# Optimization experiments

Hardware: AMD Instinct MI355X
Metric: run time of the kernel (lower is better)

Reference implementation:

```python
import jax, jax.numpy as jnp
import numpy as np

H = 16  # hidden/input size
EPS = 1e-5


def _lstm_layer(xs, W_ih, W_hh, b_ih, b_hh):
    """xs: [T, B, in]. Returns (ys [T,B,H], h_final [B,H]). PyTorch gate order i,f,g,o."""
    B = xs.shape[1]
    h0 = jnp.zeros((B, H), xs.dtype)
    c0 = jnp.zeros((B, H), xs.dtype)
    bias = b_ih + b_hh  # [4H]

    def step(carry, x_t):
        h, c = carry
        gates = x_t @ W_ih.T + h @ W_hh.T + bias  # [B, 4H]
        i, f, g, o = jnp.split(gates, 4, axis=-1)
        i = jax.nn.sigmoid(i)
        f = jax.nn.sigmoid(f)
        g = jnp.tanh(g)
        o = jax.nn.sigmoid(o)
        c = f * c + i * g
        h = o * jnp.tanh(c)
        return (h, c), h

    (h_fin, _), ys = jax.lax.scan(step, (h0, c0), xs)
    return ys, h_fin


def setup_inputs() -> dict:
    key = jax.random.key(0)
    ks = jax.random.split(key, 12)
    s = 1.0 / np.sqrt(H)  # PyTorch LSTM/Linear init scale
    B, T = 4096, 512
    x = jax.random.normal(ks[0], (B, T, H), dtype=jnp.float32)
    u = lambda k, shp: jax.random.uniform(k, shp, jnp.float32, -s, s)
    return {
        "x": x,
        "W_ih0": u(ks[1], (4 * H, H)), "W_hh0": u(ks[2], (4 * H, H)),
        "b_ih0": u(ks[3], (4 * H,)), "b_hh0": u(ks[4], (4 * H,)),
        "W_ih1": u(ks[5], (4 * H, H)), "W_hh1": u(ks[6], (4 * H, H)),
        "b_ih1": u(ks[7], (4 * H,)), "b_hh1": u(ks[8], (4 * H,)),
        "W_proj": u(ks[9], (H, H)), "b_proj": u(ks[10], (H,)),
        "ln_gamma": jnp.ones((H,), jnp.float32), "ln_beta": jnp.zeros((H,), jnp.float32),
    }


def reference(x, W_ih0, W_hh0, b_ih0, b_hh0, W_ih1, W_hh1, b_ih1, b_hh1,
              W_proj, b_proj, ln_gamma, ln_beta):
    xs = jnp.transpose(x, (1, 0, 2))  # [T, B, H] time-major for scan
    ys, _ = _lstm_layer(xs, W_ih0, W_hh0, b_ih0, b_hh0)
    _, h_n = _lstm_layer(ys, W_ih1, W_hh1, b_ih1, b_hh1)  # h_n[-1] == layer-2 final h
    z = h_n @ W_proj.T + b_proj  # [B, H]
    mu = jnp.mean(z, axis=-1, keepdims=True)
    var = jnp.mean(jnp.square(z - mu), axis=-1, keepdims=True)
    z = (z - mu) * jax.lax.rsqrt(var + EPS) * ln_gamma + ln_beta
    return jnp.tanh(z)
```

## Files before the change

### kernel.cpp

```cpp
#include <hip/hip_runtime.h>
#include <cstddef>

#define HH 16
#define TT 512
#define STG 16
#define NSTG (TT / STG)
#define LOG2E 1.44269504088896340736f

typedef float v2f __attribute__((ext_vector_type(2)));
typedef float v4f __attribute__((ext_vector_type(4)));

static __device__ __forceinline__ float fexp2(float x){ return __builtin_amdgcn_exp2f(x); }
static __device__ __forceinline__ float frcp (float x){ return __builtin_amdgcn_rcpf(x); }
static __device__ __forceinline__ float frsq (float x){ return __builtin_amdgcn_rsqf(x); }

static __device__ __forceinline__ float ftanh(float c){
    return frcp(1.0f + fexp2(c * (-2.0f*LOG2E))) * 2.0f - 1.0f;
}

#if __has_builtin(__builtin_amdgcn_mov_dpp)
template<int CTRL>
static __device__ __forceinline__ float qb(float v){
    return __builtin_bit_cast(float,
        __builtin_amdgcn_mov_dpp(__builtin_bit_cast(int,v), CTRL, 0xF, 0xF, true));
}
#else
template<int CTRL>
static __device__ __forceinline__ float qb(float v){
    return __builtin_bit_cast(float,
        __builtin_amdgcn_update_dpp(0, __builtin_bit_cast(int,v), CTRL, 0xF, 0xF, true));
}
#endif

static __device__ __forceinline__ v2f pkfma(v2f a, v2f b, v2f c){
    return __builtin_elementwise_fma(a, b, c);
}

static __device__ __forceinline__ void dot16_acc(const v4f* a, const v4f* w, v2f& s0, v2f& s1){
    s0 = pkfma(a[0].lo, w[0].lo, s0);  s1 = pkfma(a[0].hi, w[0].hi, s1);
    s0 = pkfma(a[1].lo, w[1].lo, s0);  s1 = pkfma(a[1].hi, w[1].hi, s1);
    s0 = pkfma(a[2].lo, w[2].lo, s0);  s1 = pkfma(a[2].hi, w[2].hi, s1);
    s0 = pkfma(a[3].lo, w[3].lo, s0);  s1 = pkfma(a[3].hi, w[3].hi, s1);
}

static __device__ __forceinline__ void ld4(v4f* dst, const float* p){
    const v4f* q = (const v4f*)p;
    dst[0] = q[0]; dst[1] = q[1]; dst[2] = q[2]; dst[3] = q[3];
}

__global__ __launch_bounds__(256, 4) void lstm_fused_kernel(
    const float* __restrict__ x,
    const float* __restrict__ W_ih0, const float* __restrict__ W_hh0,
    const float* __restrict__ b_ih0, const float* __restrict__ b_hh0,
    const float* __restrict__ W_ih1, const float* __restrict__ W_hh1,
    const float* __restrict__ b_ih1, const float* __restrict__ b_hh1,
    const float* __restrict__ W_proj, const float* __restrict__ b_proj,
    const float* __restrict__ ln_g, const float* __restrict__ ln_b,
    float* __restrict__ out)
{
    const int lane = threadIdx.x & 63;
    const int wave = threadIdx.x >> 6;
    const int b    = blockIdx.x * 4 + wave;

    const int g   = lane & 3;
    const int k   = lane >> 2;
    const int row = g * HH + k;

    __shared__ float sh[4 * 544];
    float* xb0 = sh + wave * 544;
    float* xb1 = xb0 + 256;
    float* h1w = xb1 + 256;
    float* h2w = h1w + 16;

    const bool  isg   = (g == 2);
    const float sc_in = isg ? (-2.0f * LOG2E) : (-LOG2E);

    v4f wih0[4], whh0[4], wih1[4], whh1[4];
#pragma unroll
    for (int q = 0; q < 4; ++q) {
        wih0[q] = ((const v4f*)(W_ih0 + row * HH))[q] * sc_in;
        whh0[q] = ((const v4f*)(W_hh0 + row * HH))[q] * sc_in;
        wih1[q] = ((const v4f*)(W_ih1 + row * HH))[q] * sc_in;
        whh1[q] = ((const v4f*)(W_hh1 + row * HH))[q] * sc_in;
    }
    const float bias0 = (b_ih0[row] + b_hh0[row]) * sc_in;
    const float bias1 = (b_ih1[row] + b_hh1[row]) * sc_in;

    const float* xg = x + (size_t)b * TT * HH;

    v4f xs = *(const v4f*)(xg + lane * 4);
    *(v4f*)(xb0 + lane * 4) = xs;
    xs = *(const v4f*)(xg + 256 + lane * 4);

    v4f xa[4];
    ld4(xa, xb0);

    float cs1, cs2 = 0.0f;
    v4f h1a[4], h2a[4];
#pragma unroll
    for (int q = 0; q < 4; ++q) h2a[q] = (v4f)(0.f);

    {
        v2f p0 = {bias0, 0.f}, p1 = {0.f, 0.f};
        dot16_acc(xa, wih0, p0, p1);
        v2f ps = p0 + p1;
        float a1 = ps.x + ps.y;
        float r1 = frcp(1.0f + fexp2(a1));
        float i1 = qb<0x00>(r1), g1 = qb<0xAA>(r1), o1 = qb<0xFF>(r1);
        float gs1 = __builtin_fmaf(g1, -4.0f*LOG2E, 2.0f*LOG2E);
        cs1 = i1 * gs1;
        float h1n = o1 * (frcp(1.0f + fexp2(cs1)) * 2.0f - 1.0f);
        h1w[k] = h1n;
        ld4(h1a, h1w);
        ld4(xa, xb0 + HH);
    }

    for (int s = 0; s < NSTG; ++s) {
        float* cur = (s & 1) ? xb1 : xb0;
        float* nxt = (s & 1) ? xb0 : xb1;

        *(v4f*)(nxt + lane * 4) = xs;
        const int sp = (s + 2 < NSTG) ? (s + 2) : (NSTG - 1);
        xs = *(const v4f*)(xg + (size_t)sp * 256 + lane * 4);

#pragma unroll
        for (int ti = 0; ti < STG; ++ti) {
            v2f p0 = {bias0, 0.f}, p1 = {0.f, 0.f};
            dot16_acc(xa, wih0, p0, p1);
            dot16_acc(h1a, whh0, p0, p1);
            v2f ps = p0 + p1;
            float a1 = ps.x + ps.y;
            float r1 = frcp(1.0f + fexp2(a1));
            float i1 = qb<0x00>(r1), f1 = qb<0x55>(r1);
            float g1 = qb<0xAA>(r1), o1 = qb<0xFF>(r1);
            float gs1 = __builtin_fmaf(g1, -4.0f*LOG2E, 2.0f*LOG2E);
            cs1 = __builtin_fmaf(f1, cs1, i1 * gs1);
            float h1n = o1 * (frcp(1.0f + fexp2(cs1)) * 2.0f - 1.0f);
            h1w[k] = h1n;

            v2f q0 = {bias1, 0.f}, q1 = {0.f, 0.f};
            dot16_acc(h1a, wih1, q0, q1);

            ld4(h1a, h1w);
            ld4(xa, (ti <= 13) ? (cur + (ti + 2) * HH) : (nxt + (ti - 14) * HH));

            dot16_acc(h2a, whh1, q0, q1);
            v2f qs = q0 + q1;
            float a2 = qs.x + qs.y;
            float r2 = frcp(1.0f + fexp2(a2));
            float i2 = qb<0x00>(r2), f2 = qb<0x55>(r2);
            float g2 = qb<0xAA>(r2), o2 = qb<0xFF>(r2);
            float gs2 = __builtin_fmaf(g2, -4.0f*LOG2E, 2.0f*LOG2E);
            cs2 = __builtin_fmaf(f2, cs2, i2 * gs2);
            float h2n = o2 * (frcp(1.0f + fexp2(cs2)) * 2.0f - 1.0f);
            h2w[k] = h2n;
            ld4(h2a, h2w);
        }
    }

    const int u = lane & 15;
    v4f wp[4];
#pragma unroll
    for (int q = 0; q < 4; ++q) wp[q] = ((const v4f*)(W_proj + u * HH))[q];
    v2f z0 = {0.f, 0.f}, z1 = {0.f, 0.f};
    dot16_acc(h2a, wp, z0, z1);
    v2f zs = z0 + z1;
    float z = b_proj[u] + zs.x + zs.y;

    float sacc = z;
    sacc += __shfl_xor(sacc, 1); sacc += __shfl_xor(sacc, 2);
    sacc += __shfl_xor(sacc, 4); sacc += __shfl_xor(sacc, 8);
    const float mu = sacc * (1.0f / 16.0f);

    const float d = z - mu;
    float q2 = d * d;
    q2 += __shfl_xor(q2, 1); q2 += __shfl_xor(q2, 2);
    q2 += __shfl_xor(q2, 4); q2 += __shfl_xor(q2, 8);
    const float var = q2 * (1.0f / 16.0f);

    const float rs  = frsq(var + 1e-5f);
    const float y   = d * rs * ln_g[u] + ln_b[u];
    const float res = ftanh(y);

    if (lane < 16) out[(size_t)b * HH + lane] = res;
}

extern "C" void kernel_launch(void* const* d_in, const int* in_sizes, int n_in,
                              void* d_out, int out_size, void* d_ws, size_t ws_size,
                              hipStream_t stream) {
    const float* x      = (const float*)d_in[0];
    const float* W_ih0  = (const float*)d_in[1];
    const float* W_hh0  = (const float*)d_in[2];
    const float* b_ih0  = (const float*)d_in[3];
    const float* b_hh0  = (const float*)d_in[4];
    const float* W_ih1  = (const float*)d_in[5];
    const float* W_hh1  = (const float*)d_in[6];
    const float* b_ih1  = (const float*)d_in[7];
    const float* b_hh1  = (const float*)d_in[8];
    const float* W_proj = (const float*)d_in[9];
    const float* b_proj = (const float*)d_in[10];
    const float* ln_g   = (const float*)d_in[11];
    const float* ln_b   = (const float*)d_in[12];
    float* out = (float*)d_out;

    const int B = in_sizes[0] / (TT * HH);
    dim3 grid(B / 4), block(256);
    hipLaunchKernelGGL(lstm_fused_kernel, grid, block, 0, stream,
                       x, W_ih0, W_hh0, b_ih0, b_hh0,
                       W_ih1, W_hh1, b_ih1, b_hh1,
                       W_proj, b_proj, ln_g, ln_b, out);
}
```

Baseline: 472.2 us.

## Process two batch sequences per wave to interleave independent LSTM recurrences

Each wavefront now advances two batch elements' two-layer LSTM recurrences in lockstep, doubling shared-memory staging and register state per wave and halving the grid. The goal is to fill the long serial dependency chain of each timestep (dot products, exp/rcp, DPP broadcasts, LDS round trips) with independent work from the second sequence. In exchange, register pressure rises (launch bounds lowered) and the number of resident waves per SIMD drops, so latency hiding shifts from wave switching to in-wave ILP.

Result: no change. 478.8 us (+1.4%).

```diff
diff --git a/kernel.cpp b/kernel.cpp
--- a/kernel.cpp
+++ b/kernel.cpp
@@ -48,7 +48,7 @@
     dst[0] = q[0]; dst[1] = q[1]; dst[2] = q[2]; dst[3] = q[3];
 }
 
-__global__ __launch_bounds__(256, 4) void lstm_fused_kernel(
+__global__ __launch_bounds__(256, 2) void lstm_fused_kernel(
     const float* __restrict__ x,
     const float* __restrict__ W_ih0, const float* __restrict__ W_hh0,
     const float* __restrict__ b_ih0, const float* __restrict__ b_hh0,
@@ -60,17 +60,20 @@
 {
     const int lane = threadIdx.x & 63;
     const int wave = threadIdx.x >> 6;
-    const int b    = blockIdx.x * 4 + wave;
+    const int bA   = blockIdx.x * 8 + wave * 2;
+    const int bB   = bA + 1;
 
     const int g   = lane & 3;
     const int k   = lane >> 2;
     const int row = g * HH + k;
 
-    __shared__ float sh[4 * 544];
-    float* xb0 = sh + wave * 544;
-    float* xb1 = xb0 + 256;
-    float* h1w = xb1 + 256;
-    float* h2w = h1w + 16;
+    __shared__ float sh[8 * 544];
+    float* shA  = sh + (wave * 2 + 0) * 544;
+    float* shB  = sh + (wave * 2 + 1) * 544;
+    float* xb0A = shA;        float* xb0B = shB;
+    float* xb1A = shA + 256;  float* xb1B = shB + 256;
+    float* h1wA = shA + 512;  float* h1wB = shB + 512;
+    float* h2wA = shA + 528;  float* h2wB = shB + 528;
 
     const bool  isg   = (g == 2);
     const float sc_in = isg ? (-2.0f * LOG2E) : (-LOG2E);
@@ -86,75 +89,112 @@
     const float bias0 = (b_ih0[row] + b_hh0[row]) * sc_in;
     const float bias1 = (b_ih1[row] + b_hh1[row]) * sc_in;
 
-    const float* xg = x + (size_t)b * TT * HH;
-
-    v4f xs = *(const v4f*)(xg + lane * 4);
-    *(v4f*)(xb0 + lane * 4) = xs;
-    xs = *(const v4f*)(xg + 256 + lane * 4);
-
-    v4f xa[4];
-    ld4(xa, xb0);
-
-    float cs1, cs2 = 0.0f;
-    v4f h1a[4], h2a[4];
-#pragma unroll
-    for (int q = 0; q < 4; ++q) h2a[q] = (v4f)(0.f);
+    const float* xgA = x + (size_t)bA * TT * HH;
+    const float* xgB = x + (size_t)bB * TT * HH;
+
+    v4f xsA = *(const v4f*)(xgA + lane * 4);
+    v4f xsB = *(const v4f*)(xgB + lane * 4);
+    *(v4f*)(xb0A + lane * 4) = xsA;
+    *(v4f*)(xb0B + lane * 4) = xsB;
+    xsA = *(const v4f*)(xgA + 256 + lane * 4);
+    xsB = *(const v4f*)(xgB + 256 + lane * 4);
+
+    v4f xaA[4], xaB[4];
+    ld4(xaA, xb0A);
+    ld4(xaB, xb0B);
+
+    float cs1A, cs2A = 0.0f;
+    float cs1B, cs2B = 0.0f;
+    v4f h1aA[4], h2aA[4], h1aB[4], h2aB[4];
+#pragma unroll
+    for (int q = 0; q < 4; ++q) { h2aA[q] = (v4f)(0.f); h2aB[q] = (v4f)(0.f); }
 
     {
-        v2f p0 = {bias0, 0.f}, p1 = {0.f, 0.f};
-        dot16_acc(xa, wih0, p0, p1);
-        v2f ps = p0 + p1;
-        float a1 = ps.x + ps.y;
-        float r1 = frcp(1.0f + fexp2(a1));
-        float i1 = qb<0x00>(r1), g1 = qb<0xAA>(r1), o1 = qb<0xFF>(r1);
-        float gs1 = __builtin_fmaf(g1, -4.0f*LOG2E, 2.0f*LOG2E);
-        cs1 = i1 * gs1;
-        float h1n = o1 * (frcp(1.0f + fexp2(cs1)) * 2.0f - 1.0f);
-        h1w[k] = h1n;
-        ld4(h1a, h1w);
-        ld4(xa, xb0 + HH);
+        v2f p0A = {bias0, 0.f}, p1A = {0.f, 0.f};
+        v2f p0B = {bias0, 0.f}, p1B = {0.f, 0.f};
+        dot16_acc(xaA, wih0, p0A, p1A);
+        dot16_acc(xaB, wih0, p0B, p1B);
+        v2f psA = p0A + p1A;               v2f psB = p0B + p1B;
+        float a1A = psA.x + psA.y;         float a1B = psB.x + psB.y;
+        float r1A = frcp(1.0f + fexp2(a1A));
+        float r1B = frcp(1.0f + fexp2(a1B));
+        float i1A = qb<0x00>(r1A), g1A = qb<0xAA>(r1A), o1A = qb<0xFF>(r1A);
+        float i1B = qb<0x00>(r1B), g1B = qb<0xAA>(r1B), o1B = qb<0xFF>(r1B);
+        float gs1A = __builtin_fmaf(g1A, -4.0f*LOG2E, 2.0f*LOG2E);
+        float gs1B = __builtin_fmaf(g1B, -4.0f*LOG2E, 2.0f*LOG2E);
+        cs1A = i1A * gs1A;                 cs1B = i1B * gs1B;
+        float h1nA = o1A * (frcp(1.0f + fexp2(cs1A)) * 2.0f - 1.0f);
+        float h1nB = o1B * (frcp(1.0f + fexp2(cs1B)) * 2.0f - 1.0f);
+        h1wA[k] = h1nA;                    h1wB[k] = h1nB;
+        ld4(h1aA, h1wA);                   ld4(h1aB, h1wB);
+        ld4(xaA, xb0A + HH);               ld4(xaB, xb0B + HH);
     }
 
     for (int s = 0; s < NSTG; ++s) {
-        float* cur = (s & 1) ? xb1 : xb0;
-        float* nxt = (s & 1) ? xb0 : xb1;
-
-        *(v4f*)(nxt + lane * 4) = xs;
+        float* curA = (s & 1) ? xb1A : xb0A;  float* nxtA = (s & 1) ? xb0A : xb1A;
+        float* curB = (s & 1) ? xb1B : xb0B;  float* nxtB = (s & 1) ? xb0B : xb1B;
+
+        *(v4f*)(nxtA + lane * 4) = xsA;
+        *(v4f*)(nxtB + lane * 4) = xsB;
         const int sp = (s + 2 < NSTG) ? (s + 2) : (NSTG - 1);
-        xs = *(const v4f*)(xg + (size_t)sp * 256 + lane * 4);
+        xsA = *(const v4f*)(xgA + (size_t)sp * 256 + lane * 4);
+        xsB = *(const v4f*)(xgB + (size_t)sp * 256 + lane * 4);
 
 #pragma unroll
         for (int ti = 0; ti < STG; ++ti) {
-            v2f p0 = {bias0, 0.f}, p1 = {0.f, 0.f};
-            dot16_acc(xa, wih0, p0, p1);
-            dot16_acc(h1a, whh0, p0, p1);
-            v2f ps = p0 + p1;
-            float a1 = ps.x + ps.y;
-            float r1 = frcp(1.0f + fexp2(a1));
-            float i1 = qb<0x00>(r1), f1 = qb<0x55>(r1);
-            float g1 = qb<0xAA>(r1), o1 = qb<0xFF>(r1);
-            float gs1 = __builtin_fmaf(g1, -4.0f*LOG2E, 2.0f*LOG2E);
-            cs1 = __builtin_fmaf(f1, cs1, i1 * gs1);
-            float h1n = o1 * (frcp(1.0f + fexp2(cs1)) * 2.0f - 1.0f);
-            h1w[k] = h1n;
-
-            v2f q0 = {bias1, 0.f}, q1 = {0.f, 0.f};
-            dot16_acc(h1a, wih1, q0, q1);
-
-            ld4(h1a, h1w);
-            ld4(xa, (ti <= 13) ? (cur + (ti + 2) * HH) : (nxt + (ti - 14) * HH));
-
-            dot16_acc(h2a, whh1, q0, q1);
-            v2f qs = q0 + q1;
-            float a2 = qs.x + qs.y;
-            float r2 = frcp(1.0f + fexp2(a2));
-            float i2 = qb<0x00>(r2), f2 = qb<0x55>(r2);
-            float g2 = qb<0xAA>(r2), o2 = qb<0xFF>(r2);
-            float gs2 = __builtin_fmaf(g2, -4.0f*LOG2E, 2.0f*LOG2E);
-            cs2 = __builtin_fmaf(f2, cs2, i2 * gs2);
-            float h2n = o2 * (frcp(1.0f + fexp2(cs2)) * 2.0f - 1.0f);
-            h2w[k] = h2n;
-            ld4(h2a, h2w);
+            v2f p0A = {bias0, 0.f}, p1A = {0.f, 0.f};
+            v2f p0B = {bias0, 0.f}, p1B = {0.f, 0.f};
+            dot16_acc(xaA, wih0, p0A, p1A);
+            dot16_acc(xaB, wih0, p0B, p1B);
+            dot16_acc(h1aA, whh0, p0A, p1A);
+            dot16_acc(h1aB, whh0, p0B, p1B);
+            v2f psA = p0A + p1A;              v2f psB = p0B + p1B;
+            float a1A = psA.x + psA.y;        float a1B = psB.x + psB.y;
+            float r1A = frcp(1.0f + fexp2(a1A));
+            float r1B = frcp(1.0f + fexp2(a1B));
+            float i1A = qb<0x00>(r1A), f1A = qb<0x55>(r1A);
+            float g1A = qb<0xAA>(r1A), o1A = qb<0xFF>(r1A);
+            float i1B = qb<0x00>(r1B), f1B = qb<0x55>(r1B);
+            float g1B = qb<0xAA>(r1B), o1B = qb<0xFF>(r1B);
+            float gs1A = __builtin_fmaf(g1A, -4.0f*LOG2E, 2.0f*LOG2E);
+            float gs1B = __builtin_fmaf(g1B, -4.0f*LOG2E, 2.0f*LOG2E);
+            cs1A = __builtin_fmaf(f1A, cs1A, i1A * gs1A);
+            cs1B = __builtin_fmaf(f1B, cs1B, i1B * gs1B);
+            float h1nA = o1A * (frcp(1.0f + fexp2(cs1A)) * 2.0f - 1.0f);
+            float h1nB = o1B * (frcp(1.0f + fexp2(cs1B)) * 2.0f - 1.0f);
+            h1wA[k] = h1nA;
+            h1wB[k] = h1nB;
+
+            v2f q0A = {bias1, 0.f}, q1A = {0.f, 0.f};
+            v2f q0B = {bias1, 0.f}, q1B = {0.f, 0.f};
+            dot16_acc(h1aA, wih1, q0A, q1A);
+            dot16_acc(h1aB, wih1, q0B, q1B);
+
+            ld4(h1aA, h1wA);
+            ld4(h1aB, h1wB);
+            ld4(xaA, (ti <= 13) ? (curA + (ti + 2) * HH) : (nxtA + (ti - 14) * HH));
+            ld4(xaB, (ti <= 13) ? (curB + (ti + 2) * HH) : (nxtB + (ti - 14) * HH));
+
+            dot16_acc(h2aA, whh1, q0A, q1A);
+            dot16_acc(h2aB, whh1, q0B, q1B);
+            v2f qsA = q0A + q1A;              v2f qsB = q0B + q1B;
+            float a2A = qsA.x + qsA.y;        float a2B = qsB.x + qsB.y;
+            float r2A = frcp(1.0f + fexp2(a2A));
+            float r2B = frcp(1.0f + fexp2(a2B));
+            float i2A = qb<0x00>(r2A), f2A = qb<0x55>(r2A);
+            float g2A = qb<0xAA>(r2A), o2A = qb<0xFF>(r2A);
+            float i2B = qb<0x00>(r2B), f2B = qb<0x55>(r2B);
+            float g2B = qb<0xAA>(r2B), o2B = qb<0xFF>(r2B);
+            float gs2A = __builtin_fmaf(g2A, -4.0f*LOG2E, 2.0f*LOG2E);
+            float gs2B = __builtin_fmaf(g2B, -4.0f*LOG2E, 2.0f*LOG2E);
+            cs2A = __builtin_fmaf(f2A, cs2A, i2A * gs2A);
+            cs2B = __builtin_fmaf(f2B, cs2B, i2B * gs2B);
+            float h2nA = o2A * (frcp(1.0f + fexp2(cs2A)) * 2.0f - 1.0f);
+            float h2nB = o2B * (frcp(1.0f + fexp2(cs2B)) * 2.0f - 1.0f);
+            h2wA[k] = h2nA;
+            h2wB[k] = h2nB;
+            ld4(h2aA, h2wA);
+            ld4(h2aB, h2wB);
         }
     }
 
@@ -162,27 +202,41 @@
     v4f wp[4];
 #pragma unroll
     for (int q = 0; q < 4; ++q) wp[q] = ((const v4f*)(W_proj + u * HH))[q];
-    v2f z0 = {0.f, 0.f}, z1 = {0.f, 0.f};
-    dot16_acc(h2a, wp, z0, z1);
-    v2f zs = z0 + z1;
-    float z = b_proj[u] + zs.x + zs.y;
-
-    float sacc = z;
-    sacc += __shfl_xor(sacc, 1); sacc += __shfl_xor(sacc, 2);
-    sacc += __shfl_xor(sacc, 4); sacc += __shfl_xor(sacc, 8);
-    const float mu = sacc * (1.0f / 16.0f);
-
-    const float d = z - mu;
-    float q2 = d * d;
-    q2 += __shfl_xor(q2, 1); q2 += __shfl_xor(q2, 2);
-    q2 += __shfl_xor(q2, 4); q2 += __shfl_xor(q2, 8);
-    const float var = q2 * (1.0f / 16.0f);
-
-    const float rs  = frsq(var + 1e-5f);
-    const float y   = d * rs * ln_g[u] + ln_b[u];
-    const float res = ftanh(y);
-
-    if (lane < 16) out[(size_t)b * HH + lane] = res;
+    const float lg = ln_g[u], lb = ln_b[u], bp = b_proj[u];
+
+    v2f z0A = {0.f, 0.f}, z1A = {0.f, 0.f};
+    v2f z0B = {0.f, 0.f}, z1B = {0.f, 0.f};
+    dot16_acc(h2aA, wp, z0A, z1A);
+    dot16_acc(h2aB, wp, z0B, z1B);
+    v2f zsA = z0A + z1A;                 v2f zsB = z0B + z1B;
+    float zA = bp + zsA.x + zsA.y;       float zB = bp + zsB.x + zsB.y;
+
+    float sA = zA, sB = zB;
+    sA += __shfl_xor(sA, 1); sB += __shfl_xor(sB, 1);
+    sA += __shfl_xor(sA, 2); sB += __shfl_xor(sB, 2);
+    sA += __shfl_xor(sA, 4); sB += __shfl_xor(sB, 4);
+    sA += __shfl_xor(sA, 8); sB += __shfl_xor(sB, 8);
+    const float muA = sA * (1.0f / 16.0f);
+    const float muB = sB * (1.0f / 16.0f);
+
+    const float dA = zA - muA;           const float dB = zB - muB;
+    float qA = dA * dA, qB = dB * dB;
+    qA += __shfl_xor(qA, 1); qB += __shfl_xor(qB, 1);
+    qA += __shfl_xor(qA, 2); qB += __shfl_xor(qB, 2);
+    qA += __shfl_xor(qA, 4); qB += __shfl_xor(qB, 4);
+    qA += __shfl_xor(qA, 8); qB += __shfl_xor(qB, 8);
+    const float varA = qA * (1.0f / 16.0f);
+    const float varB = qB * (1.0f / 16.0f);
+
+    const float yA = dA * frsq(varA + 1e-5f) * lg + lb;
+    const float yB = dB * frsq(varB + 1e-5f) * lg + lb;
+    const float resA = ftanh(yA);
+    const float resB = ftanh(yB);
+
+    if (lane < 16) {
+        out[(size_t)bA * HH + lane] = resA;
+        out[(size_t)bB * HH + lane] = resB;
+    }
 }
 
 extern "C" void kernel_launch(void* const* d_in, const int* in_sizes, int n_in,
@@ -204,7 +258,7 @@
     float* out = (float*)d_out;
 
     const int B = in_sizes[0] / (TT * HH);
-    dim3 grid(B / 4), block(256);
+    dim3 grid(B / 8), block(256);
     hipLaunchKernelGGL(lstm_fused_kernel, grid, block, 0, stream,
                        x, W_ih0, W_hh0, b_ih0, b_hh0,
                        W_ih1, W_hh1, b_ih1, b_hh1,
```

## Use one wave per block and prefetch x directly into registers

Applied to the files above, without the earlier changes.

Each block now holds a single 64-lane wave handling one batch row, where before four waves shared a 256-thread block. The shared-memory staging of x is gone: every lane loads the needed x_t vector straight from global memory into double-buffered registers, reading three steps ahead, and the loop is unrolled by two. The aim is to drop LDS traffic and staging bookkeeping and give the scheduler more freedom. In exchange, all 64 lanes issue redundant global loads of the same 64 bytes each step, there is more register pressure, and launch bounds change to (64,3).

After: 505.8 us. 1.07x slower.

```diff
diff --git a/kernel.cpp b/kernel.cpp
--- a/kernel.cpp
+++ b/kernel.cpp
@@ -3,8 +3,6 @@
 
 #define HH 16
 #define TT 512
-#define STG 16
-#define NSTG (TT / STG)
 #define LOG2E 1.44269504088896340736f
 
 typedef float v2f __attribute__((ext_vector_type(2)));
@@ -48,7 +46,44 @@
     dst[0] = q[0]; dst[1] = q[1]; dst[2] = q[2]; dst[3] = q[3];
 }
 
-__global__ __launch_bounds__(256, 4) void lstm_fused_kernel(
+#define STEP(XU, T) do {                                                     \
+                                          \
+    v2f p0 = {bias0, 0.f}, p1 = {0.f, 0.f};                                  \
+    dot16_acc(XU, wih0, p0, p1);                                             \
+    dot16_acc(h1a, whh0, p0, p1);                                            \
+    v2f ps = p0 + p1;                                                        \
+    float a1 = ps.x + ps.y;                                                  \
+    float r1 = frcp(1.0f + fexp2(a1));                                       \
+    float i1 = qb<0x00>(r1), f1 = qb<0x55>(r1);                              \
+    float g1 = qb<0xAA>(r1), o1 = qb<0xFF>(r1);                              \
+    float gs1 = __builtin_fmaf(g1, -4.0f*LOG2E, 2.0f*LOG2E);                 \
+    cs1 = __builtin_fmaf(f1, cs1, i1 * gs1);                                 \
+    float h1n = o1 * (frcp(1.0f + fexp2(cs1)) * 2.0f - 1.0f);                \
+    h1w[k] = h1n;                                       \
+              \
+    v2f q0 = {bias1, 0.f}, q1 = {0.f, 0.f};                                  \
+    dot16_acc(h1a, wih1, q0, q1);                                            \
+    ld4(h1a, h1w);                        \
+             \
+    {                                                                        \
+        const int jn = ((T) + 3 < TT) ? ((T) + 3) : (TT - 1);                \
+        ld4(XU, xg + (size_t)jn * HH);                                       \
+    }                                                                        \
+                              \
+    dot16_acc(h2a, whh1, q0, q1);                                            \
+    v2f qs = q0 + q1;                                                        \
+    float a2 = qs.x + qs.y;                                                  \
+    float r2 = frcp(1.0f + fexp2(a2));                                       \
+    float i2 = qb<0x00>(r2), f2 = qb<0x55>(r2);                              \
+    float g2 = qb<0xAA>(r2), o2 = qb<0xFF>(r2);                              \
+    float gs2 = __builtin_fmaf(g2, -4.0f*LOG2E, 2.0f*LOG2E);                 \
+    cs2 = __builtin_fmaf(f2, cs2, i2 * gs2);                                 \
+    float h2n = o2 * (frcp(1.0f + fexp2(cs2)) * 2.0f - 1.0f);                \
+    h2w[k] = h2n;                                         \
+    ld4(h2a, h2w);                         \
+} while (0)
+
+__global__ __launch_bounds__(64, 3) void lstm_fused_kernel(
     const float* __restrict__ x,
     const float* __restrict__ W_ih0, const float* __restrict__ W_hh0,
     const float* __restrict__ b_ih0, const float* __restrict__ b_hh0,
@@ -58,19 +93,16 @@
     const float* __restrict__ ln_g, const float* __restrict__ ln_b,
     float* __restrict__ out)
 {
-    const int lane = threadIdx.x & 63;
-    const int wave = threadIdx.x >> 6;
-    const int b    = blockIdx.x * 4 + wave;
+    const int lane = threadIdx.x;
+    const int b    = blockIdx.x;
 
     const int g   = lane & 3;
     const int k   = lane >> 2;
     const int row = g * HH + k;
 
-    __shared__ float sh[4 * 544];
-    float* xb0 = sh + wave * 544;
-    float* xb1 = xb0 + 256;
-    float* h1w = xb1 + 256;
-    float* h2w = h1w + 16;
+    __shared__ float sh[64];
+    float* h1w = sh;
+    float* h2w = sh + 32;
 
     const bool  isg   = (g == 2);
     const float sc_in = isg ? (-2.0f * LOG2E) : (-LOG2E);
@@ -88,12 +120,10 @@
 
     const float* xg = x + (size_t)b * TT * HH;
 
-    v4f xs = *(const v4f*)(xg + lane * 4);
-    *(v4f*)(xb0 + lane * 4) = xs;
-    xs = *(const v4f*)(xg + 256 + lane * 4);
-
-    v4f xa[4];
-    ld4(xa, xb0);
+    v4f x0[4], xbA[4], xbB[4];
+    ld4(x0,  xg);
+    ld4(xbA, xg + 1 * HH);
+    ld4(xbB, xg + 2 * HH);
 
     float cs1, cs2 = 0.0f;
     v4f h1a[4], h2a[4];
@@ -102,7 +132,7 @@
 
     {
         v2f p0 = {bias0, 0.f}, p1 = {0.f, 0.f};
-        dot16_acc(xa, wih0, p0, p1);
+        dot16_acc(x0, wih0, p0, p1);
         v2f ps = p0 + p1;
         float a1 = ps.x + ps.y;
         float r1 = frcp(1.0f + fexp2(a1));
@@ -112,50 +142,11 @@
         float h1n = o1 * (frcp(1.0f + fexp2(cs1)) * 2.0f - 1.0f);
         h1w[k] = h1n;
         ld4(h1a, h1w);
-        ld4(xa, xb0 + HH);
     }
 
-    for (int s = 0; s < NSTG; ++s) {
-        float* cur = (s & 1) ? xb1 : xb0;
-        float* nxt = (s & 1) ? xb0 : xb1;
-
-        *(v4f*)(nxt + lane * 4) = xs;
-        const int sp = (s + 2 < NSTG) ? (s + 2) : (NSTG - 1);
-        xs = *(const v4f*)(xg + (size_t)sp * 256 + lane * 4);
-
-#pragma unroll
-        for (int ti = 0; ti < STG; ++ti) {
-            v2f p0 = {bias0, 0.f}, p1 = {0.f, 0.f};
-            dot16_acc(xa, wih0, p0, p1);
-            dot16_acc(h1a, whh0, p0, p1);
-            v2f ps = p0 + p1;
-            float a1 = ps.x + ps.y;
-            float r1 = frcp(1.0f + fexp2(a1));
-            float i1 = qb<0x00>(r1), f1 = qb<0x55>(r1);
-            float g1 = qb<0xAA>(r1), o1 = qb<0xFF>(r1);
-            float gs1 = __builtin_fmaf(g1, -4.0f*LOG2E, 2.0f*LOG2E);
-            cs1 = __builtin_fmaf(f1, cs1, i1 * gs1);
-            float h1n = o1 * (frcp(1.0f + fexp2(cs1)) * 2.0f - 1.0f);
-            h1w[k] = h1n;
-
-            v2f q0 = {bias1, 0.f}, q1 = {0.f, 0.f};
-            dot16_acc(h1a, wih1, q0, q1);
-
-            ld4(h1a, h1w);
-            ld4(xa, (ti <= 13) ? (cur + (ti + 2) * HH) : (nxt + (ti - 14) * HH));
-
-            dot16_acc(h2a, whh1, q0, q1);
-            v2f qs = q0 + q1;
-            float a2 = qs.x + qs.y;
-            float r2 = frcp(1.0f + fexp2(a2));
-            float i2 = qb<0x00>(r2), f2 = qb<0x55>(r2);
-            float g2 = qb<0xAA>(r2), o2 = qb<0xFF>(r2);
-            float gs2 = __builtin_fmaf(g2, -4.0f*LOG2E, 2.0f*LOG2E);
-            cs2 = __builtin_fmaf(f2, cs2, i2 * gs2);
-            float h2n = o2 * (frcp(1.0f + fexp2(cs2)) * 2.0f - 1.0f);
-            h2w[k] = h2n;
-            ld4(h2a, h2w);
-        }
+    for (int t = 0; t < TT; t += 2) {
+        STEP(xbA, t);
+        STEP(xbB, t + 1);
     }
 
     const int u = lane & 15;
@@ -204,7 +195,7 @@
     float* out = (float*)d_out;
 
     const int B = in_sizes[0] / (TT * HH);
-    dim3 grid(B / 4), block(256);
+    dim3 grid(B), block(64);
     hipLaunchKernelGGL(lstm_fused_kernel, grid, block, 0, stream,
                        x, W_ih0, W_hh0, b_ih0, b_hh0,
                        W_ih1, W_hh1, b_ih1, b_hh1,
```
